# Kernel optimization log

Measured on AMD Instinct MI355X. Metric: run time of the kernel, lower is better.

Reference implementation:

```python
import jax, jax.numpy as jnp
import numpy as np

N, F, H, C, B = 50000, 128, 128, 32, 512
E = 600000


def _norm_edges(edge_index, n):
    # PyG GCNConv default: add self-loops, symmetric normalization
    src = jnp.concatenate([edge_index[0], jnp.arange(n, dtype=edge_index.dtype)])
    dst = jnp.concatenate([edge_index[1], jnp.arange(n, dtype=edge_index.dtype)])
    deg = jax.ops.segment_sum(jnp.ones_like(dst, dtype=jnp.float32), dst, num_segments=n)
    inv_sqrt = jnp.where(deg > 0, jax.lax.rsqrt(jnp.maximum(deg, 1.0)), 0.0)
    norm = inv_sqrt[src] * inv_sqrt[dst]  # [E+N]
    return src, dst, norm


def _gcn_conv(x, W, b, src, dst, norm, n):
    h = x @ W                                  # [N, H] dense transform
    msg = norm[:, None] * h[src]               # gather + per-edge scale
    out = jax.ops.segment_sum(msg, dst, num_segments=n)  # scatter-add
    return out + b


def setup_inputs() -> dict:
    key = jax.random.key(0)
    ks = jax.random.split(key, 20)
    x = jax.random.normal(ks[0], (N, F), dtype=jnp.float32)
    edge_index = jax.random.randint(ks[1], (2, E), 0, N, dtype=jnp.int64)
    batch = jnp.sort(jax.random.randint(ks[2], (N,), 0, B, dtype=jnp.int64))
    d = {"x": x, "edge_index": edge_index, "batch": batch}
    dims_in = [F, H, H, H, H, H]
    for i in range(6):
        s = 1.0 / np.sqrt(dims_in[i])
        d[f"W{i+1}"] = jax.random.uniform(ks[3 + i], (dims_in[i], H), jnp.float32, -s, s)
        d[f"b{i+1}"] = jnp.zeros((H,), jnp.float32)
    s = 1.0 / np.sqrt(H)
    d["lin_W"] = jax.random.uniform(ks[10], (H, C), jnp.float32, -s, s)
    d["lin_b"] = jnp.zeros((C,), jnp.float32)
    return d


def reference(x, edge_index, batch, W1, b1, W2, b2, W3, b3, W4, b4, W5, b5, W6, b6, lin_W, lin_b):
    n = x.shape[0]
    src, dst, norm = _norm_edges(edge_index, n)
    Ws = [W1, W2, W3, W4, W5, W6]
    bs = [b1, b2, b3, b4, b5, b6]
    h = x
    for i in range(6):
        h = _gcn_conv(h, Ws[i], bs[i], src, dst, norm, n)
        if i < 5:
            h = jax.nn.relu(h)
    # global mean pool over graph ids
    counts = jax.ops.segment_sum(jnp.ones((n,), jnp.float32), batch, num_segments=B)
    pooled = jax.ops.segment_sum(h, batch, num_segments=B) / jnp.maximum(counts, 1.0)[:, None]
    # dropout is identity in eval mode
    return pooled @ lin_W + lin_b
```

## Files before the change

kernel.cpp:

```cpp
#include <hip/hip_runtime.h>
#include <hip/hip_fp16.h>


static inline int ceil_div(int a, int b) { return (a + b - 1) / b; }


__global__ __launch_bounds__(256) void hist_i32(const int* __restrict__ idx,
                                                int* __restrict__ cnt, int n) {
  int i = blockIdx.x * 256 + threadIdx.x;
  if (i < n) atomicAdd(&cnt[idx[i]], 1);
}

__global__ __launch_bounds__(256) void inv_sqrt_deg(const int* __restrict__ deg,
                                                    float* __restrict__ inv, int n) {
  int i = blockIdx.x * 256 + threadIdx.x;
  if (i < n) inv[i] = rsqrtf((float)(deg[i] + 1));
}

__global__ __launch_bounds__(256) void scanA(const int* __restrict__ deg,
                                             int* __restrict__ tmp,
                                             int* __restrict__ sums, int n) {
  __shared__ int s[256];
  int t = threadIdx.x;
  int gid = blockIdx.x * 256 + t;
  s[t] = (gid < n) ? deg[gid] : 0;
  __syncthreads();
  for (int off = 1; off < 256; off <<= 1) {
    int add = (t >= off) ? s[t - off] : 0;
    __syncthreads();
    s[t] += add;
    __syncthreads();
  }
  if (gid < n) tmp[gid] = s[t];
  if (t == 255) sums[blockIdx.x] = s[255];
}

__global__ __launch_bounds__(256) void scanB(int* __restrict__ sums, int nchunk) {
  __shared__ int s[256];
  int t = threadIdx.x;
  s[t] = (t < nchunk) ? sums[t] : 0;
  __syncthreads();
  for (int off = 1; off < 256; off <<= 1) {
    int add = (t >= off) ? s[t - off] : 0;
    __syncthreads();
    s[t] += add;
    __syncthreads();
  }
  if (t < nchunk) sums[t] = s[t];
}

__global__ __launch_bounds__(256) void scanC(const int* __restrict__ tmp,
                                             const int* __restrict__ sums,
                                             int* __restrict__ rp, int n) {
  int gid = blockIdx.x * 256 + threadIdx.x;
  if (gid < n) {
    int off = (blockIdx.x > 0) ? sums[blockIdx.x - 1] : 0;
    rp[gid + 1] = tmp[gid] + off;
    if (gid == 0) rp[0] = 0;
  }
}

__global__ __launch_bounds__(256) void bsearch_starts(const int* __restrict__ batch,
                                                      int* __restrict__ gstart,
                                                      int n, int B) {
  int g = blockIdx.x * 256 + threadIdx.x;
  if (g > B) return;
  int lo = 0, hi = n;
  while (lo < hi) {
    int mid = (lo + hi) >> 1;
    if (batch[mid] < g) lo = mid + 1; else hi = mid;
  }
  gstart[g] = lo;
}

__global__ __launch_bounds__(256) void scatter_edges(const int* __restrict__ src,
                                                     const int* __restrict__ dst,
                                                     int* __restrict__ cursor,
                                                     int* __restrict__ col, int E) {
  int i = blockIdx.x * 256 + threadIdx.x;
  if (i < E) {
    int d = dst[i];
    int pos = atomicAdd(&cursor[d], 1);
    col[pos] = src[i];
  }
}


__global__ __launch_bounds__(256) void gemm_scale(const float* __restrict__ A,
                                                  const float* __restrict__ W,
                                                  const float* __restrict__ inv,
                                                  __half* __restrict__ out, int nrows) {
  __shared__ float As_t[32][68];
  __shared__ float Ws[32][128];
  int t = threadIdx.x;
  int tx = t & 15;
  int ty = t >> 4;
  int rowBase = blockIdx.x * 64;

  float acc[4][8];
#pragma unroll
  for (int i = 0; i < 4; ++i)
#pragma unroll
    for (int j = 0; j < 8; ++j) acc[i][j] = 0.f;

  for (int k0 = 0; k0 < 128; k0 += 32) {
    {
      int r = t >> 3;
      int kv = (t & 7) * 4;
#pragma unroll
      for (int p = 0; p < 2; ++p) {
        int rr = r + p * 32;
        int gr = rowBase + rr;
        int grc = (gr < nrows) ? gr : (nrows - 1);
        const float4 av = *(const float4*)&A[(size_t)grc * 128 + k0 + kv];
        As_t[kv + 0][rr] = av.x;
        As_t[kv + 1][rr] = av.y;
        As_t[kv + 2][rr] = av.z;
        As_t[kv + 3][rr] = av.w;
      }
#pragma unroll
      for (int p = 0; p < 4; ++p) {
        int idx = p * 1024 + t * 4;
        int kr = idx >> 7;
        int cc = idx & 127;
        *(float4*)&Ws[kr][cc] = *(const float4*)&W[(size_t)(k0 + kr) * 128 + cc];
      }
    }
    __syncthreads();

#pragma unroll 8
    for (int k = 0; k < 32; ++k) {
      float4 a = *(const float4*)&As_t[k][ty * 4];
      float4 w0 = *(const float4*)&Ws[k][tx * 4];
      float4 w1 = *(const float4*)&Ws[k][64 + tx * 4];
      float ar[4] = {a.x, a.y, a.z, a.w};
      float wr[8] = {w0.x, w0.y, w0.z, w0.w, w1.x, w1.y, w1.z, w1.w};
#pragma unroll
      for (int i = 0; i < 4; ++i)
#pragma unroll
        for (int j = 0; j < 8; ++j) acc[i][j] += ar[i] * wr[j];
    }
    __syncthreads();
  }

#pragma unroll
  for (int i = 0; i < 4; ++i) {
    int gr = rowBase + ty * 4 + i;
    if (gr < nrows) {
      float iv = inv[gr];
      __half2 p0 = __floats2half2_rn(acc[i][0] * iv, acc[i][1] * iv);
      __half2 p1 = __floats2half2_rn(acc[i][2] * iv, acc[i][3] * iv);
      __half2 p2 = __floats2half2_rn(acc[i][4] * iv, acc[i][5] * iv);
      __half2 p3 = __floats2half2_rn(acc[i][6] * iv, acc[i][7] * iv);
      uint2 s0, s1;
      s0.x = *(unsigned*)&p0; s0.y = *(unsigned*)&p1;
      s1.x = *(unsigned*)&p2; s1.y = *(unsigned*)&p3;
      *(uint2*)&out[(size_t)gr * 128 + tx * 4] = s0;
      *(uint2*)&out[(size_t)gr * 128 + 64 + tx * 4] = s1;
    }
  }
}

__global__ __launch_bounds__(256) void aggregate(const __half* __restrict__ hs,
                                                 const int* __restrict__ col,
                                                 const int* __restrict__ rp,
                                                 const float* __restrict__ inv,
                                                 const float* __restrict__ bias,
                                                 float* __restrict__ out, int n,
                                                 int dorelu) {
  int node = blockIdx.x * 4 + (threadIdx.x >> 6);
  if (node >= n) return;
  int lane = threadIdx.x & 63;
  const __half2* h2 = (const __half2*)hs;

  int beg = rp[node], end = rp[node + 1];
  float2 self = __half22float2(h2[(size_t)node * 64 + lane]);
  float sx[8], sy[8];
  sx[0] = self.x; sy[0] = self.y;
#pragma unroll
  for (int i = 1; i < 8; ++i) { sx[i] = 0.f; sy[i] = 0.f; }

  int e = beg;
  for (; e + 8 <= end; e += 8) {
    int idx[8];
#pragma unroll
    for (int i = 0; i < 8; ++i) idx[i] = col[e + i];
    __half2 v[8];
#pragma unroll
    for (int i = 0; i < 8; ++i) v[i] = h2[(size_t)idx[i] * 64 + lane];
#pragma unroll
    for (int i = 0; i < 8; ++i) {
      float2 f = __half22float2(v[i]);
      sx[i] += f.x; sy[i] += f.y;
    }
  }
  if (e + 4 <= end) {
    int idx[4];
#pragma unroll
    for (int i = 0; i < 4; ++i) idx[i] = col[e + i];
    __half2 v[4];
#pragma unroll
    for (int i = 0; i < 4; ++i) v[i] = h2[(size_t)idx[i] * 64 + lane];
#pragma unroll
    for (int i = 0; i < 4; ++i) {
      float2 f = __half22float2(v[i]);
      sx[i] += f.x; sy[i] += f.y;
    }
    e += 4;
  }
  for (; e < end; ++e) {
    int s = col[e];
    float2 f = __half22float2(h2[(size_t)s * 64 + lane]);
    sx[0] += f.x; sy[0] += f.y;
  }

  float ax = (sx[0] + sx[1]) + (sx[2] + sx[3]);
  float bx = (sx[4] + sx[5]) + (sx[6] + sx[7]);
  float ay = (sy[0] + sy[1]) + (sy[2] + sy[3]);
  float by = (sy[4] + sy[5]) + (sy[6] + sy[7]);

  float iv = inv[node];
  float rx = iv * (ax + bx) + bias[lane * 2 + 0];
  float ry = iv * (ay + by) + bias[lane * 2 + 1];
  if (dorelu) { rx = fmaxf(rx, 0.f); ry = fmaxf(ry, 0.f); }
  ((float2*)out)[(size_t)node * 64 + lane] = make_float2(rx, ry);
}

__global__ __launch_bounds__(128) void pool_mean(const float* __restrict__ h,
                                                 const int* __restrict__ gstart,
                                                 float* __restrict__ pooled) {
  int g = blockIdx.x;
  int c = threadIdx.x;
  int s = gstart[g], e = gstart[g + 1];
  float acc = 0.f;
  for (int v = s; v < e; ++v) acc += h[(size_t)v * 128 + c];
  int cnt = e - s;
  pooled[(size_t)g * 128 + c] = acc / (float)(cnt > 0 ? cnt : 1);
}

__global__ __launch_bounds__(256) void final_lin(const float* __restrict__ pooled,
                                                 const float* __restrict__ lw,
                                                 const float* __restrict__ lb,
                                                 float* __restrict__ out, int total) {
  int idx = blockIdx.x * 256 + threadIdx.x;
  if (idx >= total) return;
  int g = idx >> 5;
  int c = idx & 31;
  float s = 0.f;
#pragma unroll 8
  for (int k = 0; k < 128; ++k) s += pooled[(size_t)g * 128 + k] * lw[k * 32 + c];
  out[idx] = s + lb[c];
}


extern "C" void kernel_launch(void* const* d_in, const int* in_sizes, int n_in,
                              void* d_out, int out_size, void* d_ws, size_t ws_size,
                              hipStream_t stream) {
  const float* x = (const float*)d_in[0];
  const int* ei = (const int*)d_in[1];
  const int* batch = (const int*)d_in[2];
  const float* W[6];
  const float* bvec[6];
  for (int i = 0; i < 6; ++i) {
    W[i] = (const float*)d_in[3 + 2 * i];
    bvec[i] = (const float*)d_in[4 + 2 * i];
  }
  const float* linW = (const float*)d_in[15];
  const float* linb = (const float*)d_in[16];
  float* out = (float*)d_out;

  const int F = 128, H = 128, C = 32;
  const int N = in_sizes[0] / F;
  const int E = in_sizes[1] / 2;
  const int B = out_size / C;
  const int* src = ei;
  const int* dst = ei + E;

  char* w = (char*)d_ws;
  auto alloc = [&](size_t bytes) -> char* {
    char* p = w;
    w += (bytes + 255) & ~(size_t)255;
    return p;
  };
  int* deg = (int*)alloc((size_t)N * 4);
  float* inv = (float*)alloc((size_t)N * 4);
  int* tmp = (int*)alloc((size_t)N * 4);
  int* sums = (int*)alloc(256 * 4);
  int* rp = (int*)alloc((size_t)(N + 1) * 4);
  int* cursor = (int*)alloc((size_t)N * 4);
  int* col = (int*)alloc((size_t)E * 4);
  int* gstart = (int*)alloc((size_t)(B + 1) * 4);
  float* bufA = (float*)alloc((size_t)N * H * 4);
  __half* hs16 = (__half*)alloc((size_t)N * H * 2);
  float* pooled = (float*)alloc((size_t)B * H * 4);
  (void)n_in; (void)ws_size;

  hipMemsetAsync(deg, 0, (size_t)N * 4, stream);

  hist_i32<<<ceil_div(E, 256), 256, 0, stream>>>(dst, deg, E);
  inv_sqrt_deg<<<ceil_div(N, 256), 256, 0, stream>>>(deg, inv, N);

  int nchunk = ceil_div(N, 256);
  scanA<<<nchunk, 256, 0, stream>>>(deg, tmp, sums, N);
  scanB<<<1, 256, 0, stream>>>(sums, nchunk);
  scanC<<<nchunk, 256, 0, stream>>>(tmp, sums, rp, N);
  bsearch_starts<<<ceil_div(B + 1, 256), 256, 0, stream>>>(batch, gstart, N, B);

  hipMemcpyAsync(cursor, rp, (size_t)N * 4, hipMemcpyDeviceToDevice, stream);
  scatter_edges<<<ceil_div(E, 256), 256, 0, stream>>>(src, dst, cursor, col, E);

  const float* hin = x;
  for (int l = 0; l < 6; ++l) {
    gemm_scale<<<ceil_div(N, 64), 256, 0, stream>>>(hin, W[l], inv, hs16, N);
    aggregate<<<ceil_div(N, 4), 256, 0, stream>>>(hs16, col, rp, inv, bvec[l], bufA, N,
                                                  (l < 5) ? 1 : 0);
    hin = bufA;
  }

  pool_mean<<<B, 128, 0, stream>>>(bufA, gstart, pooled);
  final_lin<<<ceil_div(B * C, 256), 256, 0, stream>>>(pooled, linW, linb, out, B * C);
}
```

Measured before the change: 568.1 us.

## Use fp16 MFMA GEMM and keep activations in half precision between layers

Replaces the FP32 SIMT tiled GEMM with a matrix-core kernel built on mfma_f32_16x16x32_f16. Operands are loaded straight from global memory, with weights pre-transposed and converted to fp16 once per call. The aggregate kernel now writes fp16 activations, and pooling reads fp16, which halves the activation traffic between layers. The cost is extra rounding of inputs, weights and activations to fp16, plus two small conversion kernels. Output stores are scalar 16-bit writes, which may be poorly coalesced.

Result: faster. 535.1 us (-5.8%).

```diff
diff --git a/kernel.cpp b/kernel.cpp
--- a/kernel.cpp
+++ b/kernel.cpp
@@ -3,6 +3,10 @@
 
 
 static inline int ceil_div(int a, int b) { return (a + b - 1) / b; }
+
+typedef _Float16 f16x8 __attribute__((ext_vector_type(8)));
+typedef _Float16 f16x4 __attribute__((ext_vector_type(4)));
+typedef float f32x4 __attribute__((ext_vector_type(4)));
 
 
 __global__ __launch_bounds__(256) void hist_i32(const int* __restrict__ idx,
@@ -85,78 +89,68 @@
   }
 }
 
-
-__global__ __launch_bounds__(256) void gemm_scale(const float* __restrict__ A,
-                                                  const float* __restrict__ W,
-                                                  const float* __restrict__ inv,
-                                                  __half* __restrict__ out, int nrows) {
-  __shared__ float As_t[32][68];
-  __shared__ float Ws[32][128];
-  int t = threadIdx.x;
-  int tx = t & 15;
-  int ty = t >> 4;
-  int rowBase = blockIdx.x * 64;
-
-  float acc[4][8];
-#pragma unroll
-  for (int i = 0; i < 4; ++i)
-#pragma unroll
-    for (int j = 0; j < 8; ++j) acc[i][j] = 0.f;
-
-  for (int k0 = 0; k0 < 128; k0 += 32) {
-    {
-      int r = t >> 3;
-      int kv = (t & 7) * 4;
-#pragma unroll
-      for (int p = 0; p < 2; ++p) {
-        int rr = r + p * 32;
-        int gr = rowBase + rr;
-        int grc = (gr < nrows) ? gr : (nrows - 1);
-        const float4 av = *(const float4*)&A[(size_t)grc * 128 + k0 + kv];
-        As_t[kv + 0][rr] = av.x;
-        As_t[kv + 1][rr] = av.y;
-        As_t[kv + 2][rr] = av.z;
-        As_t[kv + 3][rr] = av.w;
-      }
-#pragma unroll
-      for (int p = 0; p < 4; ++p) {
-        int idx = p * 1024 + t * 4;
-        int kr = idx >> 7;
-        int cc = idx & 127;
-        *(float4*)&Ws[kr][cc] = *(const float4*)&W[(size_t)(k0 + kr) * 128 + cc];
-      }
-    }
-    __syncthreads();
-
-#pragma unroll 8
-    for (int k = 0; k < 32; ++k) {
-      float4 a = *(const float4*)&As_t[k][ty * 4];
-      float4 w0 = *(const float4*)&Ws[k][tx * 4];
-      float4 w1 = *(const float4*)&Ws[k][64 + tx * 4];
-      float ar[4] = {a.x, a.y, a.z, a.w};
-      float wr[8] = {w0.x, w0.y, w0.z, w0.w, w1.x, w1.y, w1.z, w1.w};
-#pragma unroll
-      for (int i = 0; i < 4; ++i)
-#pragma unroll
-        for (int j = 0; j < 8; ++j) acc[i][j] += ar[i] * wr[j];
-    }
-    __syncthreads();
-  }
-
-#pragma unroll
-  for (int i = 0; i < 4; ++i) {
-    int gr = rowBase + ty * 4 + i;
-    if (gr < nrows) {
-      float iv = inv[gr];
-      __half2 p0 = __floats2half2_rn(acc[i][0] * iv, acc[i][1] * iv);
-      __half2 p1 = __floats2half2_rn(acc[i][2] * iv, acc[i][3] * iv);
-      __half2 p2 = __floats2half2_rn(acc[i][4] * iv, acc[i][5] * iv);
-      __half2 p3 = __floats2half2_rn(acc[i][6] * iv, acc[i][7] * iv);
-      uint2 s0, s1;
-      s0.x = *(unsigned*)&p0; s0.y = *(unsigned*)&p1;
-      s1.x = *(unsigned*)&p2; s1.y = *(unsigned*)&p3;
-      *(uint2*)&out[(size_t)gr * 128 + tx * 4] = s0;
-      *(uint2*)&out[(size_t)gr * 128 + 64 + tx * 4] = s1;
+__global__ __launch_bounds__(256) void f32_to_f16(const float* __restrict__ in,
+                                                  _Float16* __restrict__ out, int n) {
+  int i = (blockIdx.x * 256 + threadIdx.x) * 4;
+  if (i < n) {
+    float4 v = *(const float4*)&in[i];
+    f16x4 o = {(_Float16)v.x, (_Float16)v.y, (_Float16)v.z, (_Float16)v.w};
+    *(f16x4*)&out[i] = o;
+  }
+}
+
+struct WP { const float* p[6]; };
+__global__ __launch_bounds__(256) void conv_weights(WP wp, _Float16* __restrict__ wt) {
+  int wi = blockIdx.x >> 6;
+  int e = (blockIdx.x & 63) * 256 + threadIdx.x;
+  int k = e >> 7, c = e & 127;
+  wt[((size_t)wi << 14) + (size_t)c * 128 + k] = (_Float16)wp.p[wi][e];
+}
+
+
+__global__ __launch_bounds__(256) void gemm_mfma(const _Float16* __restrict__ A,
+                                                 const _Float16* __restrict__ Wt,
+                                                 const float* __restrict__ inv,
+                                                 _Float16* __restrict__ out, int nrows) {
+  int lane = threadIdx.x & 63;
+  int wv = threadIdx.x >> 6;
+  int rowBase = blockIdx.x * 64 + wv * 16;
+  int r = lane & 15, g = lane >> 4;
+
+  int arow = rowBase + r;
+  if (arow >= nrows) arow = nrows - 1;
+  const _Float16* ap = A + (size_t)arow * 128 + g * 8;
+  f16x8 a0 = *(const f16x8*)(ap + 0);
+  f16x8 a1 = *(const f16x8*)(ap + 32);
+  f16x8 a2 = *(const f16x8*)(ap + 64);
+  f16x8 a3 = *(const f16x8*)(ap + 96);
+
+  f32x4 acc[8];
+#pragma unroll
+  for (int ct = 0; ct < 8; ++ct) acc[ct] = (f32x4){0.f, 0.f, 0.f, 0.f};
+
+  const _Float16* bp = Wt + (size_t)r * 128 + g * 8;
+#pragma unroll
+  for (int ct = 0; ct < 8; ++ct) {
+    const _Float16* bt = bp + (size_t)ct * 16 * 128;
+    f16x8 b0 = *(const f16x8*)(bt + 0);
+    f16x8 b1 = *(const f16x8*)(bt + 32);
+    f16x8 b2 = *(const f16x8*)(bt + 64);
+    f16x8 b3 = *(const f16x8*)(bt + 96);
+    acc[ct] = __builtin_amdgcn_mfma_f32_16x16x32_f16(a0, b0, acc[ct], 0, 0, 0);
+    acc[ct] = __builtin_amdgcn_mfma_f32_16x16x32_f16(a1, b1, acc[ct], 0, 0, 0);
+    acc[ct] = __builtin_amdgcn_mfma_f32_16x16x32_f16(a2, b2, acc[ct], 0, 0, 0);
+    acc[ct] = __builtin_amdgcn_mfma_f32_16x16x32_f16(a3, b3, acc[ct], 0, 0, 0);
+  }
+
+#pragma unroll
+  for (int j = 0; j < 4; ++j) {
+    int row = rowBase + g * 4 + j;
+    if (row < nrows) {
+      float iv = inv[row];
+#pragma unroll
+      for (int ct = 0; ct < 8; ++ct)
+        out[(size_t)row * 128 + ct * 16 + r] = (_Float16)(acc[ct][j] * iv);
     }
   }
 }
@@ -166,7 +160,7 @@
                                                  const int* __restrict__ rp,
                                                  const float* __restrict__ inv,
                                                  const float* __restrict__ bias,
-                                                 float* __restrict__ out, int n,
+                                                 __half* __restrict__ out, int n,
                                                  int dorelu) {
   int node = blockIdx.x * 4 + (threadIdx.x >> 6);
   if (node >= n) return;
@@ -223,17 +217,17 @@
   float rx = iv * (ax + bx) + bias[lane * 2 + 0];
   float ry = iv * (ay + by) + bias[lane * 2 + 1];
   if (dorelu) { rx = fmaxf(rx, 0.f); ry = fmaxf(ry, 0.f); }
-  ((float2*)out)[(size_t)node * 64 + lane] = make_float2(rx, ry);
-}
-
-__global__ __launch_bounds__(128) void pool_mean(const float* __restrict__ h,
+  ((__half2*)out)[(size_t)node * 64 + lane] = __floats2half2_rn(rx, ry);
+}
+
+__global__ __launch_bounds__(128) void pool_mean(const __half* __restrict__ h,
                                                  const int* __restrict__ gstart,
                                                  float* __restrict__ pooled) {
   int g = blockIdx.x;
   int c = threadIdx.x;
   int s = gstart[g], e = gstart[g + 1];
   float acc = 0.f;
-  for (int v = s; v < e; ++v) acc += h[(size_t)v * 128 + c];
+  for (int v = s; v < e; ++v) acc += __half2float(h[(size_t)v * 128 + c]);
   int cnt = e - s;
   pooled[(size_t)g * 128 + c] = acc / (float)(cnt > 0 ? cnt : 1);
 }
@@ -259,10 +253,10 @@
   const float* x = (const float*)d_in[0];
   const int* ei = (const int*)d_in[1];
   const int* batch = (const int*)d_in[2];
-  const float* W[6];
+  WP wp;
   const float* bvec[6];
   for (int i = 0; i < 6; ++i) {
-    W[i] = (const float*)d_in[3 + 2 * i];
+    wp.p[i] = (const float*)d_in[3 + 2 * i];
     bvec[i] = (const float*)d_in[4 + 2 * i];
   }
   const float* linW = (const float*)d_in[15];
@@ -290,8 +284,9 @@
   int* cursor = (int*)alloc((size_t)N * 4);
   int* col = (int*)alloc((size_t)E * 4);
   int* gstart = (int*)alloc((size_t)(B + 1) * 4);
-  float* bufA = (float*)alloc((size_t)N * H * 4);
-  __half* hs16 = (__half*)alloc((size_t)N * H * 2);
+  _Float16* h16 = (_Float16*)alloc((size_t)N * H * 2);
+  _Float16* hs16 = (_Float16*)alloc((size_t)N * H * 2);
+  _Float16* wt16 = (_Float16*)alloc((size_t)6 * H * H * 2);
   float* pooled = (float*)alloc((size_t)B * H * 4);
   (void)n_in; (void)ws_size;
 
@@ -309,14 +304,17 @@
   hipMemcpyAsync(cursor, rp, (size_t)N * 4, hipMemcpyDeviceToDevice, stream);
   scatter_edges<<<ceil_div(E, 256), 256, 0, stream>>>(src, dst, cursor, col, E);
 
-  const float* hin = x;
+  f32_to_f16<<<ceil_div(N * F / 4, 256), 256, 0, stream>>>(x, h16, N * F);
+  conv_weights<<<384, 256, 0, stream>>>(wp, wt16);
+
   for (int l = 0; l < 6; ++l) {
-    gemm_scale<<<ceil_div(N, 64), 256, 0, stream>>>(hin, W[l], inv, hs16, N);
-    aggregate<<<ceil_div(N, 4), 256, 0, stream>>>(hs16, col, rp, inv, bvec[l], bufA, N,
+    gemm_mfma<<<ceil_div(N, 64), 256, 0, stream>>>(h16, wt16 + ((size_t)l << 14), inv,
+                                                   hs16, N);
+    aggregate<<<ceil_div(N, 4), 256, 0, stream>>>((const __half*)hs16, col, rp, inv,
+                                                  bvec[l], (__half*)h16, N,
                                                   (l < 5) ? 1 : 0);
-    hin = bufA;
-  }
-
-  pool_mean<<<B, 128, 0, stream>>>(bufA, gstart, pooled);
+  }
+
+  pool_mean<<<B, 128, 0, stream>>>((const __half*)h16, gstart, pooled);
   final_lin<<<ceil_div(B * C, 256), 256, 0, stream>>>(pooled, linW, linb, out, B * C);
 }
```
